# Optimization experiments

Hardware: AMD Instinct MI355X
Metric: run time of the kernel (lower is better)

The kernel has to match this reference:

```python
import jax, jax.numpy as jnp
import numpy as np

COMMITMENT_COST = 0.25
EPSILON = 1e-05


def setup_inputs() -> dict:
    key = jax.random.key(0)
    k1, k2, k3 = jax.random.split(key, 3)
    inputs = jax.random.normal(k1, (32, 256, 32, 32), dtype=jnp.float32)
    embedding = jax.random.normal(k2, (256, 1024), dtype=jnp.float32)
    cluster_size = jax.random.uniform(k3, (1024,), dtype=jnp.float32)
    return {"inputs": inputs, "embedding": embedding, "cluster_size": cluster_size}


def reference(inputs, embedding, cluster_size):
    B = inputs.shape[0]
    D, K = embedding.shape  # (embedding_dim, num_embeddings)

    # Faithful to source: reshape (B,C,H,W) -> (-1, D) WITHOUT permuting.
    flat_input = inputs.reshape(-1, D)  # (N, D), N = B*H*W (since C == D)

    distances = (
        jnp.sum(flat_input ** 2, axis=1, keepdims=True)
        + jnp.sum(embedding ** 2, axis=0, keepdims=True)
        - 2.0 * flat_input @ embedding
    )  # (N, K)
    encoding_indices = jnp.argmin(distances, axis=1)  # (N,)

    # Gather codes: embedding[:, idx].T -> (N, D), reshape back to input shape
    quantized = jnp.take(embedding, encoding_indices, axis=1).T.reshape(inputs.shape)

    e_latent_loss = jnp.mean((jax.lax.stop_gradient(quantized) - inputs) ** 2)
    q_latent_loss = jnp.mean((quantized - jax.lax.stop_gradient(inputs)) ** 2)
    commitment_loss = COMMITMENT_COST * q_latent_loss
    vq_loss = e_latent_loss + commitment_loss

    # Straight-through estimator
    quantized_ste = inputs + jax.lax.stop_gradient(quantized - inputs)

    avg_probs = cluster_size / (jnp.sum(cluster_size) + EPSILON)
    perplexity = jnp.exp(-jnp.sum(avg_probs * jnp.log(avg_probs + EPSILON)))
    used_codes = jnp.sum((cluster_size > EPSILON).astype(jnp.float32))
    code_usage_rate = used_codes / K

    return (quantized_ste, vq_loss, perplexity, code_usage_rate,
            encoding_indices.reshape(B, -1))
```

## Files before the change

kernel.cpp:

```cpp
#include <hip/hip_runtime.h>


constexpr int DIM = 256;
constexpr int NK  = 1024;
constexpr int RR  = 16;
constexpr int NG  = DIM / 4;

#define GLL16(GSRC, LDST)                                                      \
  __builtin_amdgcn_global_load_lds(                                            \
      (const __attribute__((address_space(1))) void*)(GSRC),                   \
      (__attribute__((address_space(3))) void*)(LDST), 16, 0, 0)

__global__ __launch_bounds__(256) void enorm_kernel(
    const float* __restrict__ emb, float* __restrict__ enorm) {
  int k = blockIdx.x * 256 + threadIdx.x;
  float s = 0.f;
  for (int d = 0; d < DIM; ++d) {
    float e = emb[(size_t)d * NK + k];
    s = fmaf(e, e, s);
  }
  enorm[k] = 0.5f * s;
}

__global__ __launch_bounds__(256, 3) void argmin_kernel(
    const float* __restrict__ x, const float* __restrict__ emb,
    const float* __restrict__ enorm, int* __restrict__ idx_out,
    float* __restrict__ idx_out_f) {
  __shared__ float xs[RR * DIM];
  __shared__ float es[2][4][NK];
  __shared__ float red_v[4][RR];
  __shared__ int   red_i[4][RR];

  const int tid = threadIdx.x;
  const int k0  = tid * 4;
  const size_t xbase = (size_t)blockIdx.x * (RR * DIM);

  #pragma unroll
  for (int i = 0; i < 4; ++i)
    GLL16(x + xbase + (size_t)(tid + 256 * i) * 4, &xs[(tid + 256 * i) * 4]);
  #pragma unroll
  for (int r = 0; r < 4; ++r)
    GLL16(emb + (size_t)r * NK + k0, &es[0][r][k0]);
  __syncthreads();

  float acc[RR][4];
  #pragma unroll
  for (int r = 0; r < RR; ++r) {
    #pragma unroll
    for (int j = 0; j < 4; ++j) acc[r][j] = 0.f;
  }

  #pragma unroll 2
  for (int g = 0; g < NG; ++g) {
    if (g < NG - 1) {
      const float* src = emb + (size_t)((g + 1) * 4) * NK + k0;
      #pragma unroll
      for (int r = 0; r < 4; ++r)
        GLL16(src + (size_t)r * NK, &es[(g + 1) & 1][r][k0]);
      asm volatile("s_waitcnt vmcnt(4)" ::: "memory");
    } else {
      asm volatile("s_waitcnt vmcnt(0)" ::: "memory");
    }
    __builtin_amdgcn_sched_barrier(0);

    const int b = g & 1;
    const float4 e0 = *(const float4*)&es[b][0][k0];
    const float4 e1 = *(const float4*)&es[b][1][k0];
    const float4 e2 = *(const float4*)&es[b][2][k0];
    const float4 e3 = *(const float4*)&es[b][3][k0];
    #pragma unroll
    for (int r = 0; r < RR; ++r) {
      const float4 xv = *(const float4*)&xs[r * DIM + g * 4];
      acc[r][0] = fmaf(xv.x, e0.x, fmaf(xv.y, e1.x, fmaf(xv.z, e2.x, fmaf(xv.w, e3.x, acc[r][0]))));
      acc[r][1] = fmaf(xv.x, e0.y, fmaf(xv.y, e1.y, fmaf(xv.z, e2.y, fmaf(xv.w, e3.y, acc[r][1]))));
      acc[r][2] = fmaf(xv.x, e0.z, fmaf(xv.y, e1.z, fmaf(xv.z, e2.z, fmaf(xv.w, e3.z, acc[r][2]))));
      acc[r][3] = fmaf(xv.x, e0.w, fmaf(xv.y, e1.w, fmaf(xv.z, e2.w, fmaf(xv.w, e3.w, acc[r][3]))));
    }
  }

  const float4 en = *(const float4*)(enorm + k0);
  const int lane = tid & 63;
  const int wv   = tid >> 6;

  for (int r = 0; r < RR; ++r) {
    float bv = en.x - acc[r][0];
    int   bi = k0;
    { float v = en.y - acc[r][1]; if (v < bv) { bv = v; bi = k0 + 1; } }
    { float v = en.z - acc[r][2]; if (v < bv) { bv = v; bi = k0 + 2; } }
    { float v = en.w - acc[r][3]; if (v < bv) { bv = v; bi = k0 + 3; } }
    for (int off = 32; off > 0; off >>= 1) {
      float ov = __shfl_xor(bv, off);
      int   oi = __shfl_xor(bi, off);
      if (ov < bv || (ov == bv && oi < bi)) { bv = ov; bi = oi; }
    }
    if (lane == 0) { red_v[wv][r] = bv; red_i[wv][r] = bi; }
  }
  __syncthreads();

  if (tid < RR) {
    float bv = red_v[0][tid];
    int   bi = red_i[0][tid];
    #pragma unroll
    for (int w = 1; w < 4; ++w) {
      float v = red_v[w][tid]; int i2 = red_i[w][tid];
      if (v < bv || (v == bv && i2 < bi)) { bv = v; bi = i2; }
    }
    const int n = blockIdx.x * RR + tid;
    idx_out[n]   = bi;
    idx_out_f[n] = (float)bi;
  }
}

__global__ __launch_bounds__(256) void gather_loss_kernel(
    const float* __restrict__ x, const float* __restrict__ emb,
    const int* __restrict__ idx, float* __restrict__ out_q,
    float* __restrict__ partial) {
  const int tid = threadIdx.x;
  const size_t base = (size_t)blockIdx.x * 2048;
  float local = 0.f;
  #pragma unroll
  for (int h = 0; h < 2; ++h) {
    const size_t g = base + (size_t)h * 1024 + (size_t)tid * 4;
    const int n = (int)(g >> 8);
    const int d = (int)(g & 255);
    const int k = idx[n];
    const float* ep = emb + (size_t)d * NK + k;
    float4 q;
    q.x = ep[0]; q.y = ep[NK]; q.z = ep[2 * NK]; q.w = ep[3 * NK];
    const float4 xv = *(const float4*)(x + g);
    *(float4*)(out_q + g) = q;
    const float dx = q.x - xv.x, dy = q.y - xv.y, dz = q.z - xv.z, dw = q.w - xv.w;
    local = fmaf(dx, dx, local);
    local = fmaf(dy, dy, local);
    local = fmaf(dz, dz, local);
    local = fmaf(dw, dw, local);
  }
  for (int off = 32; off > 0; off >>= 1) local += __shfl_down(local, off);
  __shared__ float wsum[4];
  if ((tid & 63) == 0) wsum[tid >> 6] = local;
  __syncthreads();
  if (tid == 0) partial[blockIdx.x] = (wsum[0] + wsum[1]) + (wsum[2] + wsum[3]);
}

__global__ __launch_bounds__(1024) void finalize_kernel(
    const float* __restrict__ partial, int np,
    const float* __restrict__ cs, float* __restrict__ out_s,
    float inv_count) {
  __shared__ float sd[1024];
  const int tid = threadIdx.x;

  float s = 0.f;
  for (int i = tid; i < np; i += 1024) s += partial[i];
  sd[tid] = s; __syncthreads();
  for (int st = 512; st > 0; st >>= 1) {
    if (tid < st) sd[tid] += sd[tid + st];
    __syncthreads();
  }
  const float total_sq = sd[0];
  __syncthreads();

  const float c = cs[tid];
  sd[tid] = c; __syncthreads();
  for (int st = 512; st > 0; st >>= 1) {
    if (tid < st) sd[tid] += sd[tid + st];
    __syncthreads();
  }
  const float S = sd[0];
  __syncthreads();

  const float p = c / (S + 1e-5f);
  sd[tid] = p * logf(p + 1e-5f);
  __syncthreads();
  for (int st = 512; st > 0; st >>= 1) {
    if (tid < st) sd[tid] += sd[tid + st];
    __syncthreads();
  }
  const float T = sd[0];
  __syncthreads();

  sd[tid] = (c > 1e-5f) ? 1.f : 0.f;
  __syncthreads();
  for (int st = 512; st > 0; st >>= 1) {
    if (tid < st) sd[tid] += sd[tid + st];
    __syncthreads();
  }
  const float U = sd[0];

  if (tid == 0) {
    out_s[0] = 1.25f * total_sq * inv_count;
    out_s[1] = expf(-T);
    out_s[2] = U * (1.f / 1024.f);
  }
}

extern "C" void kernel_launch(void* const* d_in, const int* in_sizes, int n_in,
                              void* d_out, int out_size, void* d_ws, size_t ws_size,
                              hipStream_t stream) {
  const float* x   = (const float*)d_in[0];
  const float* emb = (const float*)d_in[1];
  const float* cs  = (const float*)d_in[2];
  float* out = (float*)d_out;

  const int N = in_sizes[0] / DIM;
  const size_t ND = (size_t)N * DIM;

  float* enorm   = (float*)d_ws;
  int*   idxw    = (int*)((char*)d_ws + NK * sizeof(float));
  float* partial = (float*)((char*)d_ws + NK * sizeof(float) + (size_t)N * sizeof(int));

  const int nGather = (int)(ND / 2048);

  enorm_kernel<<<NK / 256, 256, 0, stream>>>(emb, enorm);
  argmin_kernel<<<N / RR, 256, 0, stream>>>(x, emb, enorm, idxw, out + ND + 3);
  gather_loss_kernel<<<nGather, 256, 0, stream>>>(x, emb, idxw, out, partial);
  finalize_kernel<<<1, 1024, 0, stream>>>(partial, nGather, cs, out + ND,
                                          1.0f / (float)ND);
}
```

Baseline: 290.5 us.

## Enlarge argmin register tile to 16 rows by 8 codes per thread

Each argmin block now handles 32 rows instead of 16. Each wave computes 16 rows against 512 codes, with every thread holding a 16x8 accumulator tile split across two code halves. The x values are loaded from LDS as float4 once every two depth steps and reused from registers, and the codebook is staged per wave, two depth rows at a time. The aim is higher FMA-to-LDS-read intensity, paid for with more VGPRs and LDS, an occupancy hint lowered from 3 to 2, and duplicated embedding loads across waves.

```diff
diff --git a/kernel.cpp b/kernel.cpp
--- a/kernel.cpp
+++ b/kernel.cpp
@@ -3,8 +3,8 @@
 
 constexpr int DIM = 256;
 constexpr int NK  = 1024;
-constexpr int RR  = 16;
-constexpr int NG  = DIM / 4;
+constexpr int RR  = 32;
+constexpr int NH  = DIM / 2;
 
 #define GLL16(GSRC, LDST)                                                      \
   __builtin_amdgcn_global_load_lds(                                            \
@@ -22,72 +22,95 @@
   enorm[k] = 0.5f * s;
 }
 
-__global__ __launch_bounds__(256, 3) void argmin_kernel(
+__global__ __launch_bounds__(256, 2) void argmin_kernel(
     const float* __restrict__ x, const float* __restrict__ emb,
     const float* __restrict__ enorm, int* __restrict__ idx_out,
     float* __restrict__ idx_out_f) {
   __shared__ float xs[RR * DIM];
-  __shared__ float es[2][4][NK];
-  __shared__ float red_v[4][RR];
-  __shared__ int   red_i[4][RR];
-
-  const int tid = threadIdx.x;
-  const int k0  = tid * 4;
+  __shared__ float es[2][4][2][512];
+  __shared__ float red_v[4][16];
+  __shared__ int   red_i[4][16];
+
+  const int tid   = threadIdx.x;
+  const int lane  = tid & 63;
+  const int wv    = tid >> 6;
+  const int rbase = (wv >> 1) * 16;
+  const int c_lo  = 256 * (wv & 1) + 4 * lane;
+  const int c_hi  = c_lo + 512;
   const size_t xbase = (size_t)blockIdx.x * (RR * DIM);
 
   #pragma unroll
-  for (int i = 0; i < 4; ++i)
+  for (int i = 0; i < 8; ++i)
     GLL16(x + xbase + (size_t)(tid + 256 * i) * 4, &xs[(tid + 256 * i) * 4]);
   #pragma unroll
-  for (int r = 0; r < 4; ++r)
-    GLL16(emb + (size_t)r * NK + k0, &es[0][r][k0]);
-  __syncthreads();
-
-  float acc[RR][4];
-  #pragma unroll
-  for (int r = 0; r < RR; ++r) {
+  for (int d = 0; d < 2; ++d) {
+    GLL16(emb + (size_t)d * NK + c_lo, &es[0][wv][d][4 * lane]);
+    GLL16(emb + (size_t)d * NK + c_hi, &es[0][wv][d][256 + 4 * lane]);
+  }
+  __syncthreads();
+
+  float acc[16][8];
+  #pragma unroll
+  for (int r = 0; r < 16; ++r)
     #pragma unroll
-    for (int j = 0; j < 4; ++j) acc[r][j] = 0.f;
-  }
+    for (int j = 0; j < 8; ++j) acc[r][j] = 0.f;
+
+  float4 xv[16];
 
   #pragma unroll 2
-  for (int g = 0; g < NG; ++g) {
-    if (g < NG - 1) {
-      const float* src = emb + (size_t)((g + 1) * 4) * NK + k0;
-      #pragma unroll
-      for (int r = 0; r < 4; ++r)
-        GLL16(src + (size_t)r * NK, &es[(g + 1) & 1][r][k0]);
+  for (int h = 0; h < NH; ++h) {
+    if (h < NH - 1) {
+      const float* s0 = emb + (size_t)(2 * (h + 1)) * NK;
+      const int p = (h + 1) & 1;
+      GLL16(s0 + c_lo,      &es[p][wv][0][4 * lane]);
+      GLL16(s0 + c_hi,      &es[p][wv][0][256 + 4 * lane]);
+      GLL16(s0 + NK + c_lo, &es[p][wv][1][4 * lane]);
+      GLL16(s0 + NK + c_hi, &es[p][wv][1][256 + 4 * lane]);
       asm volatile("s_waitcnt vmcnt(4)" ::: "memory");
     } else {
       asm volatile("s_waitcnt vmcnt(0)" ::: "memory");
     }
     __builtin_amdgcn_sched_barrier(0);
 
-    const int b = g & 1;
-    const float4 e0 = *(const float4*)&es[b][0][k0];
-    const float4 e1 = *(const float4*)&es[b][1][k0];
-    const float4 e2 = *(const float4*)&es[b][2][k0];
-    const float4 e3 = *(const float4*)&es[b][3][k0];
+    const int p = h & 1;
+    const float4 el0 = *(const float4*)&es[p][wv][0][4 * lane];
+    const float4 eh0 = *(const float4*)&es[p][wv][0][256 + 4 * lane];
+    const float4 el1 = *(const float4*)&es[p][wv][1][4 * lane];
+    const float4 eh1 = *(const float4*)&es[p][wv][1][256 + 4 * lane];
+
+    if ((h & 1) == 0) {
+      #pragma unroll
+      for (int r = 0; r < 16; ++r)
+        xv[r] = *(const float4*)&xs[(rbase + r) * DIM + (h >> 1) * 4];
+    }
     #pragma unroll
-    for (int r = 0; r < RR; ++r) {
-      const float4 xv = *(const float4*)&xs[r * DIM + g * 4];
-      acc[r][0] = fmaf(xv.x, e0.x, fmaf(xv.y, e1.x, fmaf(xv.z, e2.x, fmaf(xv.w, e3.x, acc[r][0]))));
-      acc[r][1] = fmaf(xv.x, e0.y, fmaf(xv.y, e1.y, fmaf(xv.z, e2.y, fmaf(xv.w, e3.y, acc[r][1]))));
-      acc[r][2] = fmaf(xv.x, e0.z, fmaf(xv.y, e1.z, fmaf(xv.z, e2.z, fmaf(xv.w, e3.z, acc[r][2]))));
-      acc[r][3] = fmaf(xv.x, e0.w, fmaf(xv.y, e1.w, fmaf(xv.z, e2.w, fmaf(xv.w, e3.w, acc[r][3]))));
-    }
-  }
-
-  const float4 en = *(const float4*)(enorm + k0);
-  const int lane = tid & 63;
-  const int wv   = tid >> 6;
-
-  for (int r = 0; r < RR; ++r) {
-    float bv = en.x - acc[r][0];
-    int   bi = k0;
-    { float v = en.y - acc[r][1]; if (v < bv) { bv = v; bi = k0 + 1; } }
-    { float v = en.z - acc[r][2]; if (v < bv) { bv = v; bi = k0 + 2; } }
-    { float v = en.w - acc[r][3]; if (v < bv) { bv = v; bi = k0 + 3; } }
+    for (int r = 0; r < 16; ++r) {
+      const float xa = ((h & 1) == 0) ? xv[r].x : xv[r].z;
+      const float xb = ((h & 1) == 0) ? xv[r].y : xv[r].w;
+      acc[r][0] = fmaf(xa, el0.x, fmaf(xb, el1.x, acc[r][0]));
+      acc[r][1] = fmaf(xa, el0.y, fmaf(xb, el1.y, acc[r][1]));
+      acc[r][2] = fmaf(xa, el0.z, fmaf(xb, el1.z, acc[r][2]));
+      acc[r][3] = fmaf(xa, el0.w, fmaf(xb, el1.w, acc[r][3]));
+      acc[r][4] = fmaf(xa, eh0.x, fmaf(xb, eh1.x, acc[r][4]));
+      acc[r][5] = fmaf(xa, eh0.y, fmaf(xb, eh1.y, acc[r][5]));
+      acc[r][6] = fmaf(xa, eh0.z, fmaf(xb, eh1.z, acc[r][6]));
+      acc[r][7] = fmaf(xa, eh0.w, fmaf(xb, eh1.w, acc[r][7]));
+    }
+  }
+
+  const float4 enl = *(const float4*)(enorm + c_lo);
+  const float4 enh = *(const float4*)(enorm + c_hi);
+
+  for (int r = 0; r < 16; ++r) {
+    float bv = enl.x - acc[r][0];
+    int   bi = c_lo;
+    { float v = enl.y - acc[r][1]; if (v < bv) { bv = v; bi = c_lo + 1; } }
+    { float v = enl.z - acc[r][2]; if (v < bv) { bv = v; bi = c_lo + 2; } }
+    { float v = enl.w - acc[r][3]; if (v < bv) { bv = v; bi = c_lo + 3; } }
+    { float v = enh.x - acc[r][4]; if (v < bv) { bv = v; bi = c_hi; } }
+    { float v = enh.y - acc[r][5]; if (v < bv) { bv = v; bi = c_hi + 1; } }
+    { float v = enh.z - acc[r][6]; if (v < bv) { bv = v; bi = c_hi + 2; } }
+    { float v = enh.w - acc[r][7]; if (v < bv) { bv = v; bi = c_hi + 3; } }
     for (int off = 32; off > 0; off >>= 1) {
       float ov = __shfl_xor(bv, off);
       int   oi = __shfl_xor(bi, off);
@@ -97,14 +120,13 @@
   }
   __syncthreads();
 
-  if (tid < RR) {
-    float bv = red_v[0][tid];
-    int   bi = red_i[0][tid];
-    #pragma unroll
-    for (int w = 1; w < 4; ++w) {
-      float v = red_v[w][tid]; int i2 = red_i[w][tid];
-      if (v < bv || (v == bv && i2 < bi)) { bv = v; bi = i2; }
-    }
+  if (tid < 32) {
+    const int row = tid & 15;
+    const int w0  = (tid >> 4) * 2;
+    float bv = red_v[w0][row];
+    int   bi = red_i[w0][row];
+    { float v = red_v[w0 + 1][row]; int i2 = red_i[w0 + 1][row];
+      if (v < bv || (v == bv && i2 < bi)) { bv = v; bi = i2; } }
     const int n = blockIdx.x * RR + tid;
     idx_out[n]   = bi;
     idx_out_f[n] = (float)bi;
```

Result: slower. 1.039 ms (+257.7%).

## Load input rows straight to registers with double-buffered software pipeline in argmin

Applied to the files above, without the earlier changes.

The argmin kernel no longer stages the 16 input rows in shared memory. Each thread now reads them directly from global memory into two register buffers, loading the next group while the current one is computed. The loop is manually unrolled by two, with explicit waitcnt and schedule barriers to overlap the embedding tile staging with the FMA work. This removes the upfront shared-memory x staging and the per-iteration LDS reads of x. In exchange it needs many more registers (128 for the x buffers), and the launch bound drops from 3 to 2 blocks per SIMD, which lowers occupancy.

```diff
diff --git a/kernel.cpp b/kernel.cpp
--- a/kernel.cpp
+++ b/kernel.cpp
@@ -4,7 +4,6 @@
 constexpr int DIM = 256;
 constexpr int NK  = 1024;
 constexpr int RR  = 16;
-constexpr int NG  = DIM / 4;
 
 #define GLL16(GSRC, LDST)                                                      \
   __builtin_amdgcn_global_load_lds(                                            \
@@ -22,65 +21,87 @@
   enorm[k] = 0.5f * s;
 }
 
-__global__ __launch_bounds__(256, 3) void argmin_kernel(
+#define STAGE(G, P)                                                            \
+  { const float* _s = emb + ((size_t)(4 * (G)) << 10) + k0;                    \
+    GLL16(_s,          &es[(P)][0][k0]);                                       \
+    GLL16(_s + NK,     &es[(P)][1][k0]);                                       \
+    GLL16(_s + 2 * NK, &es[(P)][2][k0]);                                       \
+    GLL16(_s + 3 * NK, &es[(P)][3][k0]); }
+
+#define XLOAD(XA, G)                                                           \
+  _Pragma("unroll")                                                            \
+  for (int r = 0; r < RR; ++r)                                                 \
+    XA[r] = *(const float4*)&xg[r * DIM + 4 * (G)];
+
+#define COMPUTE4(PAR, XA)                                                      \
+  { const float4 e0 = *(const float4*)&es[(PAR)][0][k0];                       \
+    const float4 e1 = *(const float4*)&es[(PAR)][1][k0];                       \
+    const float4 e2 = *(const float4*)&es[(PAR)][2][k0];                       \
+    const float4 e3 = *(const float4*)&es[(PAR)][3][k0];                       \
+    _Pragma("unroll")                                                          \
+    for (int r = 0; r < RR; ++r) {                                             \
+      const float4 xv = XA[r];                                                 \
+      acc[r][0] = fmaf(xv.x, e0.x, fmaf(xv.y, e1.x, fmaf(xv.z, e2.x, fmaf(xv.w, e3.x, acc[r][0])))); \
+      acc[r][1] = fmaf(xv.x, e0.y, fmaf(xv.y, e1.y, fmaf(xv.z, e2.y, fmaf(xv.w, e3.y, acc[r][1])))); \
+      acc[r][2] = fmaf(xv.x, e0.z, fmaf(xv.y, e1.z, fmaf(xv.z, e2.z, fmaf(xv.w, e3.z, acc[r][2])))); \
+      acc[r][3] = fmaf(xv.x, e0.w, fmaf(xv.y, e1.w, fmaf(xv.z, e2.w, fmaf(xv.w, e3.w, acc[r][3])))); \
+    } }
+
+#define SB __builtin_amdgcn_sched_barrier(0);
+
+__global__ __launch_bounds__(256, 2) void argmin_kernel(
     const float* __restrict__ x, const float* __restrict__ emb,
     const float* __restrict__ enorm, int* __restrict__ idx_out,
     float* __restrict__ idx_out_f) {
-  __shared__ float xs[RR * DIM];
   __shared__ float es[2][4][NK];
   __shared__ float red_v[4][RR];
   __shared__ int   red_i[4][RR];
 
-  const int tid = threadIdx.x;
-  const int k0  = tid * 4;
-  const size_t xbase = (size_t)blockIdx.x * (RR * DIM);
-
-  #pragma unroll
-  for (int i = 0; i < 4; ++i)
-    GLL16(x + xbase + (size_t)(tid + 256 * i) * 4, &xs[(tid + 256 * i) * 4]);
-  #pragma unroll
-  for (int r = 0; r < 4; ++r)
-    GLL16(emb + (size_t)r * NK + k0, &es[0][r][k0]);
-  __syncthreads();
+  const int tid  = threadIdx.x;
+  const int lane = tid & 63;
+  const int wv   = tid >> 6;
+  const int k0   = tid * 4;
+  const float* xg = x + (size_t)blockIdx.x * (RR * DIM);
+
+  STAGE(0, 0)
+  STAGE(1, 1)
+  asm volatile("s_waitcnt vmcnt(4)" ::: "memory");
+  SB
+
+  float4 xA[RR], xB[RR];
+  XLOAD(xA, 0)
 
   float acc[RR][4];
   #pragma unroll
-  for (int r = 0; r < RR; ++r) {
+  for (int r = 0; r < RR; ++r)
     #pragma unroll
     for (int j = 0; j < 4; ++j) acc[r][j] = 0.f;
-  }
-
-  #pragma unroll 2
-  for (int g = 0; g < NG; ++g) {
-    if (g < NG - 1) {
-      const float* src = emb + (size_t)((g + 1) * 4) * NK + k0;
-      #pragma unroll
-      for (int r = 0; r < 4; ++r)
-        GLL16(src + (size_t)r * NK, &es[(g + 1) & 1][r][k0]);
+
+  #pragma unroll 1
+  for (int gg = 0; gg < 32; ++gg) {
+    const int g0 = 2 * gg;
+    const int g1 = g0 + 1;
+
+    asm volatile("s_waitcnt vmcnt(4)" ::: "memory");
+    SB
+    XLOAD(xB, g1)
+    COMPUTE4(0, xA)
+    SB
+    if (gg <= 30) STAGE(g0 + 2, 0)
+
+    if (gg < 31) {
       asm volatile("s_waitcnt vmcnt(4)" ::: "memory");
     } else {
       asm volatile("s_waitcnt vmcnt(0)" ::: "memory");
     }
-    __builtin_amdgcn_sched_barrier(0);
-
-    const int b = g & 1;
-    const float4 e0 = *(const float4*)&es[b][0][k0];
-    const float4 e1 = *(const float4*)&es[b][1][k0];
-    const float4 e2 = *(const float4*)&es[b][2][k0];
-    const float4 e3 = *(const float4*)&es[b][3][k0];
-    #pragma unroll
-    for (int r = 0; r < RR; ++r) {
-      const float4 xv = *(const float4*)&xs[r * DIM + g * 4];
-      acc[r][0] = fmaf(xv.x, e0.x, fmaf(xv.y, e1.x, fmaf(xv.z, e2.x, fmaf(xv.w, e3.x, acc[r][0]))));
-      acc[r][1] = fmaf(xv.x, e0.y, fmaf(xv.y, e1.y, fmaf(xv.z, e2.y, fmaf(xv.w, e3.y, acc[r][1]))));
-      acc[r][2] = fmaf(xv.x, e0.z, fmaf(xv.y, e1.z, fmaf(xv.z, e2.z, fmaf(xv.w, e3.z, acc[r][2]))));
-      acc[r][3] = fmaf(xv.x, e0.w, fmaf(xv.y, e1.w, fmaf(xv.z, e2.w, fmaf(xv.w, e3.w, acc[r][3]))));
-    }
+    SB
+    if (gg <= 30) XLOAD(xA, g1 + 1)
+    COMPUTE4(1, xB)
+    SB
+    if (gg <= 30) STAGE(g1 + 2, 1)
   }
 
   const float4 en = *(const float4*)(enorm + k0);
-  const int lane = tid & 63;
-  const int wv   = tid >> 6;
 
   for (int r = 0; r < RR; ++r) {
     float bv = en.x - acc[r][0];
```

Result: slower. 348.9 us (+20.1%).
